# Kernel tuning notes

Hardware: AMD Instinct MI355X
Metric: run time of the kernel (lower is better)

Reference implementation:

```python
import jax, jax.numpy as jnp
import numpy as np

NUM_HEADS = 12
TOPK = 4


def setup_inputs() -> dict:
    key = jax.random.key(0)
    ks = jax.random.split(key, 5)
    B, N, C = 32, 577, 768
    s = 0.02
    return {
        "x": jax.random.normal(ks[0], (B, N, C), jnp.float32),
        "qkv_w": jax.random.normal(ks[1], (3 * C, C), jnp.float32) * s,
        "qkv_b": jax.random.normal(ks[2], (3 * C,), jnp.float32) * s,
        "proj_w": jax.random.normal(ks[3], (C, C), jnp.float32) * s,
        "proj_b": jax.random.normal(ks[4], (C,), jnp.float32) * s,
    }


def reference(x, qkv_w, qkv_b, proj_w, proj_b):
    B, N, C = x.shape
    H = NUM_HEADS
    D = C // H
    scale = D ** -0.5  # 0.125, matches original_attention.scale

    # qkv projection: (B,N,3C) -> (3,B,H,N,D)
    qkv = (x @ qkv_w.T + qkv_b).reshape(B, N, 3, H, D).transpose(2, 0, 3, 1, 4)
    q, k, v = qkv[0], qkv[1], qkv[2]

    # heuristic head routing: mean squared query energy per head
    scores = jnp.mean(q.astype(jnp.float32) ** 2, axis=(0, 2, 3))  # (H,)
    _, idx = jax.lax.top_k(scores, TOPK)
    idx = jnp.sort(idx)  # (topk,)

    q_sel = q[:, idx]  # (B,topk,N,D)
    k_sel = k[:, idx]
    v_sel = v[:, idx]

    attn = jax.nn.softmax(jnp.einsum('bhnd,bhmd->bhnm', q_sel, k_sel) * scale, axis=-1)
    y_sel = jnp.einsum('bhnm,bhmd->bhnd', attn, v_sel)  # (B,topk,N,D)

    # scatter selected heads back into full-size tensors (as in the torch module)
    y_full = jnp.zeros((B, H, N, D), x.dtype).at[:, idx].set(y_sel)
    x_out = y_full.transpose(0, 2, 1, 3).reshape(B, N, C) @ proj_w.T + proj_b

    attn_full = jnp.zeros((B, H, N, N), x.dtype).at[:, idx].set(attn)
    return x_out, attn_full
```

## Files before the change

### kernel.cpp

```cpp
#include <hip/hip_runtime.h>
#include <hip/hip_bf16.h>
#include <stdint.h>
#include <stddef.h>

#define B_ 32
#define N_ 577
#define C_ 768
#define H_ 12
#define D_ 64
#define M_ (B_*N_)
#define K3_ (3*C_)
#define NP_ 640
#define NN_ (N_*N_)

typedef __bf16 bf16x8_t __attribute__((ext_vector_type(8)));
typedef float f32x4 __attribute__((ext_vector_type(4)));
typedef unsigned short u16x8 __attribute__((ext_vector_type(8)));
typedef unsigned short u16x4 __attribute__((ext_vector_type(4)));

static __device__ __forceinline__ f32x4 mfma16(u16x8 a, u16x8 b, f32x4 c) {
  return __builtin_amdgcn_mfma_f32_16x16x32_bf16(
      __builtin_bit_cast(bf16x8_t, a), __builtin_bit_cast(bf16x8_t, b), c, 0, 0, 0);
}

static __device__ __forceinline__ unsigned short f2bf(float x) {
  unsigned int u = __builtin_bit_cast(unsigned int, x);
  u += 0x7fffu + ((u >> 16) & 1u);
  return (unsigned short)(u >> 16);
}

static __device__ __forceinline__ void glds16(const unsigned short* g, unsigned short* l) {
  __builtin_amdgcn_global_load_lds(
      (__attribute__((address_space(1))) void*)g,
      (__attribute__((address_space(3))) void*)l,
      16, 0, 0);
}

__global__ void k_cvt(const float* __restrict__ src, unsigned short* __restrict__ dst, int n4,
                      float* __restrict__ zeroptr) {
  if (zeroptr && blockIdx.x == 0 && threadIdx.x < 16) zeroptr[threadIdx.x] = 0.f;
  int stride = gridDim.x * blockDim.x;
  for (int i = blockIdx.x * blockDim.x + threadIdx.x; i < n4; i += stride) {
    float4 v = ((const float4*)src)[i];
    u16x4 o;
    o[0] = f2bf(v.x); o[1] = f2bf(v.y); o[2] = f2bf(v.z); o[3] = f2bf(v.w);
    *(u16x4*)(dst + (size_t)i * 4) = o;
  }
}

template<int MODE>
__global__ void k_gemm(const unsigned short* __restrict__ A,
                       const unsigned short* __restrict__ Bm,
                       const float* __restrict__ bias,
                       unsigned short* __restrict__ qb,
                       unsigned short* __restrict__ kb,
                       unsigned short* __restrict__ vb,
                       float* __restrict__ scores,
                       float* __restrict__ out,
                       int Mtot, int Ktot)
{
  __shared__ unsigned short As[128 * 32];
  __shared__ unsigned short Bs[128 * 32];
  const int bm = blockIdx.x, bn = blockIdx.y;
  const int tid = threadIdx.x;
  const int w = tid >> 6, l = tid & 63;
  const int wm = w >> 1, wn = w & 1;
  const int lr = l & 15, lg = l >> 4;
  const int lk = lg * 8;
  f32x4 acc[4][4] = {};
  const int rowA0 = bm * 128, rowB0 = bn * 128;
  const int le0 = w * 1024 + l * 8;
  const int kiters = Ktot >> 5;
  for (int kt = 0; kt < kiters; ++kt) {
    __syncthreads();
    #pragma unroll
    for (int c = 0; c < 2; ++c) {
      int lea = le0 + c * 512;
      int ra = lea >> 5, ka = lea & 31;
      glds16(A  + (size_t)(rowA0 + ra) * Ktot + kt * 32 + ka, As + (w * 2 + c) * 512);
      glds16(Bm + (size_t)(rowB0 + ra) * Ktot + kt * 32 + ka, Bs + (w * 2 + c) * 512);
    }
    __syncthreads();
    u16x8 af[4], bfr[4];
    #pragma unroll
    for (int i = 0; i < 4; ++i)
      af[i] = *(const u16x8*)(As + (wm * 64 + i * 16 + lr) * 32 + lk);
    #pragma unroll
    for (int j = 0; j < 4; ++j)
      bfr[j] = *(const u16x8*)(Bs + (wn * 64 + j * 16 + lr) * 32 + lk);
    #pragma unroll
    for (int i = 0; i < 4; ++i)
      #pragma unroll
      for (int j = 0; j < 4; ++j)
        acc[i][j] = mfma16(af[i], bfr[j], acc[i][j]);
  }

  const int rbase = lg * 4;
  if (MODE == 0) {
    const int n0 = rowB0 + wn * 64;
    const int t0 = n0 / C_;
    const int h0 = (n0 % C_) >> 6;
    unsigned short* dstbuf = (t0 == 0) ? qb : ((t0 == 1) ? kb : vb);
    float bs[4];
    #pragma unroll
    for (int j = 0; j < 4; ++j) bs[j] = bias[n0 + j * 16 + lr];
    float sq = 0.f;
    #pragma unroll
    for (int i = 0; i < 4; ++i) {
      const int mbase = rowA0 + wm * 64 + i * 16 + rbase;
      const int bb0 = mbase / N_;
      const int np0 = mbase - bb0 * N_;
      #pragma unroll
      for (int r = 0; r < 4; ++r) {
        const int mm = mbase + r;
        if (mm < Mtot) {
          int np = np0 + r, bb = bb0;
          if (np >= N_) { np -= N_; bb += 1; }
          unsigned short* drow = dstbuf + (((size_t)(bb * H_ + h0)) * N_ + np) * D_;
          #pragma unroll
          for (int j = 0; j < 4; ++j) {
            const float v = acc[i][j][r] + bs[j];
            if (t0 == 0) sq += v * v;
            drow[j * 16 + lr] = f2bf(v);
          }
        }
      }
    }
    if (t0 == 0) {
      #pragma unroll
      for (int s2 = 1; s2 < 64; s2 <<= 1) sq += __shfl_xor(sq, s2);
      if (l == 0) atomicAdd(scores + h0, sq);
    }
  } else {
    #pragma unroll
    for (int j = 0; j < 4; ++j) {
      const int n = rowB0 + wn * 64 + j * 16 + lr;
      const float bsj = bias[n];
      #pragma unroll
      for (int i = 0; i < 4; ++i) {
        const int mbase = rowA0 + wm * 64 + i * 16 + rbase;
        #pragma unroll
        for (int r = 0; r < 4; ++r) {
          const int mm = mbase + r;
          if (mm < Mtot) out[(size_t)mm * C_ + n] = acc[i][j][r] + bsj;
        }
      }
    }
  }
}

__global__ void k_topk(const float* __restrict__ scores, int* __restrict__ idxp) {
  if (threadIdx.x == 0 && blockIdx.x == 0) {
    float s[H_];
    bool used[H_];
    for (int i = 0; i < H_; ++i) { s[i] = scores[i]; used[i] = false; }
    int sel[4];
    for (int t = 0; t < 4; ++t) {
      int best = 0; float bv = -3.0e38f;
      for (int i = 0; i < H_; ++i)
        if (!used[i] && s[i] > bv) { bv = s[i]; best = i; }
      used[best] = true; sel[t] = best;
    }
    for (int a = 0; a < 4; ++a)
      for (int b = a + 1; b < 4; ++b)
        if (sel[b] < sel[a]) { int t = sel[a]; sel[a] = sel[b]; sel[b] = t; }
    for (int t = 0; t < 4; ++t) idxp[t] = sel[t];
  }
}

__global__ void k_gatherpw(const float* __restrict__ pw, const int* __restrict__ idxp,
                           unsigned short* __restrict__ pwsel) {
  int i = blockIdx.x * 256 + threadIdx.x;
  if (i >= C_ * 256) return;
  int c = i >> 8, j = i & 255;
  int h = idxp[j >> 6], d = j & 63;
  pwsel[i] = f2bf(pw[(size_t)c * C_ + h * 64 + d]);
}

__global__ void k_transv(const unsigned short* __restrict__ vb, unsigned short* __restrict__ vT) {
  __shared__ unsigned short t[64][72];
  const int bid = blockIdx.x;
  const int nt = bid % 10;
  const int bh = bid / 10;
  const int n0 = nt * 64;
  const int tid = threadIdx.x;
  {
    const int r = tid >> 2, q4 = (tid & 3) * 16;
    const int n = n0 + r;
    u16x8 v0, v1;
    if (n < N_) {
      const unsigned short* src = vb + ((size_t)bh * N_ + n) * D_ + q4;
      v0 = *(const u16x8*)(src);
      v1 = *(const u16x8*)(src + 8);
    } else {
      #pragma unroll
      for (int j = 0; j < 8; ++j) { v0[j] = 0; v1[j] = 0; }
    }
    *(u16x8*)&t[r][q4] = v0;
    *(u16x8*)&t[r][q4 + 8] = v1;
  }
  __syncthreads();
  {
    const int d = tid >> 2, nc = (tid & 3) * 16;
    u16x8 w0, w1;
    #pragma unroll
    for (int j = 0; j < 8; ++j) { w0[j] = t[nc + j][d]; w1[j] = t[nc + 8 + j][d]; }
    unsigned short* dst = vT + ((size_t)bh * D_ + d) * NP_ + n0 + nc;
    *(u16x8*)(dst) = w0;
    *(u16x8*)(dst + 8) = w1;
  }
}

#define ZSEG_ 41617
__global__ void k_attn(const unsigned short* __restrict__ qb,
                       const unsigned short* __restrict__ kb,
                       const unsigned short* __restrict__ vT,
                       const int* __restrict__ idxp,
                       float* __restrict__ attn_out,
                       unsigned short* __restrict__ ysel)
{
  __shared__ unsigned short Plds[4][16][72];
  const int bid = blockIdx.x;

  if (bid >= 1280) {
    const int zbid = bid - 1280;
    const int seg = zbid & 7, zp = zbid >> 3;
    const int zb = zp >> 3, hu = zp & 7;
    const int i0 = idxp[0], i1 = idxp[1], i2 = idxp[2], i3 = idxp[3];
    int zh = 0, u = 0;
    for (int c = 0; c < H_; ++c) {
      bool sel = (c == i0) | (c == i1) | (c == i2) | (c == i3);
      if (!sel) { if (u == hu) { zh = c; break; } ++u; }
    }
    float* slab = attn_out + ((size_t)(zb * H_ + zh)) * NN_ + seg * ZSEG_;
    const int len = (seg == 7) ? (NN_ - 7 * ZSEG_) : ZSEG_;
    for (int t = threadIdx.x * 4; t < len; t += 4096) {
      #pragma unroll
      for (int j = 0; j < 4; ++j)
        if (t + j < len) slab[t + j] = 0.f;
    }
    return;
  }

  const int qt = bid >> 7;
  const int pair = bid & 127;
  const int b  = pair >> 2;
  const int hs = pair & 3;
  const int h  = idxp[hs];
  const int tid = threadIdx.x;
  const int w = tid >> 6, l = tid & 63;
  const int lr = l & 15, lg = l >> 4, lk = lg * 8;
  const float sc2 = 0.125f * 1.44269504f;

  const size_t bh = (size_t)(b * H_ + h);
  const unsigned short* qbase = qb + bh * ((size_t)N_ * D_);
  const unsigned short* kbase = kb + bh * ((size_t)N_ * D_);
  const unsigned short* vbase = vT + bh * ((size_t)D_ * NP_);
  float* aout = attn_out + bh * (size_t)NN_;

  const int qrow = qt * 64 + w * 16 + lr;
  const int qrc = (qrow < N_) ? qrow : (N_ - 1);
  u16x8 qf0 = *(const u16x8*)(qbase + (size_t)qrc * D_ + lk);
  u16x8 qf1 = *(const u16x8*)(qbase + (size_t)qrc * D_ + 32 + lk);

  float m2[4], lsum[4];
  #pragma unroll
  for (int r = 0; r < 4; ++r) { m2[r] = -1.0e30f; lsum[r] = 0.f; }

  for (int kt = 0; kt < 10; ++kt) {
    f32x4 s[4];
    bool vc[4];
    #pragma unroll
    for (int cg = 0; cg < 4; ++cg) {
      const int kc = kt * 64 + cg * 16 + lr;
      vc[cg] = (kc < N_);
      const int kcc = vc[cg] ? kc : (N_ - 1);
      const unsigned short* kp = kbase + (size_t)kcc * D_;
      u16x8 k0 = *(const u16x8*)(kp + lk);
      u16x8 k1 = *(const u16x8*)(kp + 32 + lk);
      f32x4 a = {0.f, 0.f, 0.f, 0.f};
      __builtin_amdgcn_s_setprio(1);
      a = mfma16(qf0, k0, a);
      a = mfma16(qf1, k1, a);
      __builtin_amdgcn_s_setprio(0);
      s[cg] = a;
    }
    #pragma unroll
    for (int r = 0; r < 4; ++r) {
      float tk[4];
      float mk = -1.0e30f;
      #pragma unroll
      for (int cg = 0; cg < 4; ++cg) {
        tk[cg] = vc[cg] ? s[cg][r] * sc2 : -1.0e30f;
        mk = fmaxf(mk, tk[cg]);
      }
      const float mn = fmaxf(m2[r], mk);
      float se = 0.f;
      #pragma unroll
      for (int cg = 0; cg < 4; ++cg)
        se += exp2f(tk[cg] - mn);
      lsum[r] = lsum[r] * exp2f(m2[r] - mn) + se;
      m2[r] = mn;
    }
  }
  #pragma unroll
  for (int x = 1; x < 16; x <<= 1) {
    #pragma unroll
    for (int r = 0; r < 4; ++r) {
      const float mo = __shfl_xor(m2[r], x);
      const float lo = __shfl_xor(lsum[r], x);
      const float mn = fmaxf(m2[r], mo);
      lsum[r] = lsum[r] * exp2f(m2[r] - mn) + lo * exp2f(mo - mn);
      m2[r] = mn;
    }
  }
  float off2[4];
  #pragma unroll
  for (int r = 0; r < 4; ++r) off2[r] = m2[r] + __log2f(lsum[r]);

  f32x4 y[4] = {};
  const int orow0 = qt * 64 + w * 16 + lg * 4;

  for (int kt = 0; kt < 10; ++kt) {
    f32x4 s[4];
    bool vc[4];
    #pragma unroll
    for (int cg = 0; cg < 4; ++cg) {
      const int kc = kt * 64 + cg * 16 + lr;
      vc[cg] = (kc < N_);
      const int kcc = vc[cg] ? kc : (N_ - 1);
      const unsigned short* kp = kbase + (size_t)kcc * D_;
      u16x8 k0 = *(const u16x8*)(kp + lk);
      u16x8 k1 = *(const u16x8*)(kp + 32 + lk);
      f32x4 a = {0.f, 0.f, 0.f, 0.f};
      __builtin_amdgcn_s_setprio(1);
      a = mfma16(qf0, k0, a);
      a = mfma16(qf1, k1, a);
      __builtin_amdgcn_s_setprio(0);
      s[cg] = a;
    }
    #pragma unroll
    for (int cg = 0; cg < 4; ++cg) {
      const int kc = kt * 64 + cg * 16 + lr;
      #pragma unroll
      for (int r = 0; r < 4; ++r) {
        float p = exp2f(__builtin_fmaf(s[cg][r], sc2, -off2[r]));
        p = vc[cg] ? p : 0.f;
        const int row = orow0 + r;
        if (vc[cg] && row < N_)
          aout[(size_t)row * N_ + kc] = p;
        Plds[w][lg * 4 + r][cg * 16 + lr] = f2bf(p);
      }
    }
    u16x8 pa0 = *(const u16x8*)&Plds[w][lr][lk];
    u16x8 pa1 = *(const u16x8*)&Plds[w][lr][32 + lk];
    #pragma unroll
    for (int cg2 = 0; cg2 < 4; ++cg2) {
      const unsigned short* vp = vbase + (size_t)(cg2 * 16 + lr) * NP_ + kt * 64;
      u16x8 v0 = *(const u16x8*)(vp + lk);
      u16x8 v1 = *(const u16x8*)(vp + 32 + lk);
      __builtin_amdgcn_s_setprio(1);
      y[cg2] = mfma16(pa0, v0, y[cg2]);
      y[cg2] = mfma16(pa1, v1, y[cg2]);
      __builtin_amdgcn_s_setprio(0);
    }
  }

  #pragma unroll
  for (int cg2 = 0; cg2 < 4; ++cg2)
    #pragma unroll
    for (int r = 0; r < 4; ++r) {
      const int row = orow0 + r;
      if (row < N_)
        ysel[((size_t)(b * N_ + row)) * 256 + hs * 64 + cg2 * 16 + lr] = f2bf(y[cg2][r]);
    }
}

extern "C" void kernel_launch(void* const* d_in, const int* in_sizes, int n_in,
                              void* d_out, int out_size, void* d_ws, size_t ws_size,
                              hipStream_t stream) {
  const float* x      = (const float*)d_in[0];
  const float* qkv_w  = (const float*)d_in[1];
  const float* qkv_b  = (const float*)d_in[2];
  const float* proj_w = (const float*)d_in[3];
  const float* proj_b = (const float*)d_in[4];

  float* xout = (float*)d_out;
  float* attn_out = (float*)d_out + (size_t)M_ * C_;

  char* ws = (char*)d_ws;
  size_t o = 0;
  unsigned short* xb    = (unsigned short*)(ws + o);
  unsigned short* vT    = (unsigned short*)(ws + o);
  o += 31457280;
  unsigned short* wqkvb = (unsigned short*)(ws + o); o += 3538944;
  unsigned short* qb    = (unsigned short*)(ws + o); o += 28360704;
  unsigned short* kb    = (unsigned short*)(ws + o); o += 28360704;
  unsigned short* vb    = (unsigned short*)(ws + o); o += 28360704;
  unsigned short* ysel  = (unsigned short*)(ws + o); o += 9453568;
  unsigned short* pwsel = (unsigned short*)(ws + o); o += 393216;
  float* scores         = (float*)(ws + o);
  int*   idxp           = (int*)(ws + o + 64);

  k_cvt<<<2048, 256, 0, stream>>>(x, xb, (M_ * C_) / 4, scores);
  k_cvt<<<1728, 256, 0, stream>>>(qkv_w, wqkvb, (K3_ * C_) / 4, nullptr);

  k_gemm<0><<<dim3(145, 18), 256, 0, stream>>>(xb, wqkvb, qkv_b,
                                               qb, kb, vb, scores, nullptr,
                                               M_, C_);

  k_topk<<<1, 64, 0, stream>>>(scores, idxp);
  k_gatherpw<<<768, 256, 0, stream>>>(proj_w, idxp, pwsel);
  k_transv<<<3840, 256, 0, stream>>>(vb, vT);

  k_attn<<<3328, 256, 0, stream>>>(qb, kb, vT, idxp, attn_out, ysel);

  k_gemm<1><<<dim3(145, 6), 256, 0, stream>>>(ysel, pwsel, proj_b,
                                              nullptr, nullptr, nullptr, nullptr, xout,
                                              M_, 256);
}
```

Measured before the change: 389.6 us.

## Move attention zero-fill into QKV GEMM and transpose only selected V heads

```diff
diff --git a/kernel.cpp b/kernel.cpp
--- a/kernel.cpp
+++ b/kernel.cpp
@@ -48,6 +48,8 @@
   }
 }
 
+#define ZROWS_ 6
+#define ZPER_ 146948
 template<int MODE>
 __global__ void k_gemm(const unsigned short* __restrict__ A,
                        const unsigned short* __restrict__ Bm,
@@ -61,8 +63,23 @@
 {
   __shared__ unsigned short As[128 * 32];
   __shared__ unsigned short Bs[128 * 32];
-  const int bm = blockIdx.x, bn = blockIdx.y;
   const int tid = threadIdx.x;
+
+  if (MODE == 0 && blockIdx.y < ZROWS_) {
+    const int zblk = blockIdx.y * 145 + blockIdx.x;
+    const size_t Z = (size_t)B_ * H_ * NN_;
+    size_t s0 = (size_t)zblk * ZPER_;
+    size_t len = ZPER_;
+    if (s0 + len > Z) len = Z - s0;
+    float* zo = out + s0;
+    const float4 z4 = {0.f, 0.f, 0.f, 0.f};
+    for (size_t t = tid * 4; t + 4 <= len; t += 4096)
+      *(float4*)(zo + t) = z4;
+    return;
+  }
+
+  const int bm = blockIdx.x;
+  const int bn = (MODE == 0) ? (blockIdx.y - ZROWS_) : blockIdx.y;
   const int w = tid >> 6, l = tid & 63;
   const int wm = w >> 1, wn = w & 1;
   const int lr = l & 15, lg = l >> 4;
@@ -177,11 +194,16 @@
   pwsel[i] = f2bf(pw[(size_t)c * C_ + h * 64 + d]);
 }
 
-__global__ void k_transv(const unsigned short* __restrict__ vb, unsigned short* __restrict__ vT) {
+__global__ void k_transv(const unsigned short* __restrict__ vb, unsigned short* __restrict__ vT,
+                         const int* __restrict__ idxp) {
   __shared__ unsigned short t[64][72];
   const int bid = blockIdx.x;
   const int nt = bid % 10;
-  const int bh = bid / 10;
+  const int p  = bid / 10;
+  const int b  = p >> 2, hs = p & 3;
+  const int h  = idxp[hs];
+  const size_t bh_src = (size_t)(b * H_ + h);
+  const size_t bh_dst = (size_t)(b * 4 + hs);
   const int n0 = nt * 64;
   const int tid = threadIdx.x;
   {
@@ -189,7 +211,7 @@
     const int n = n0 + r;
     u16x8 v0, v1;
     if (n < N_) {
-      const unsigned short* src = vb + ((size_t)bh * N_ + n) * D_ + q4;
+      const unsigned short* src = vb + (bh_src * N_ + n) * D_ + q4;
       v0 = *(const u16x8*)(src);
       v1 = *(const u16x8*)(src + 8);
     } else {
@@ -205,13 +227,12 @@
     u16x8 w0, w1;
     #pragma unroll
     for (int j = 0; j < 8; ++j) { w0[j] = t[nc + j][d]; w1[j] = t[nc + 8 + j][d]; }
-    unsigned short* dst = vT + ((size_t)bh * D_ + d) * NP_ + n0 + nc;
+    unsigned short* dst = vT + (bh_dst * D_ + d) * NP_ + n0 + nc;
     *(u16x8*)(dst) = w0;
     *(u16x8*)(dst + 8) = w1;
   }
 }
 
-#define ZSEG_ 41617
 __global__ void k_attn(const unsigned short* __restrict__ qb,
                        const unsigned short* __restrict__ kb,
                        const unsigned short* __restrict__ vT,
@@ -222,26 +243,6 @@
   __shared__ unsigned short Plds[4][16][72];
   const int bid = blockIdx.x;
 
-  if (bid >= 1280) {
-    const int zbid = bid - 1280;
-    const int seg = zbid & 7, zp = zbid >> 3;
-    const int zb = zp >> 3, hu = zp & 7;
-    const int i0 = idxp[0], i1 = idxp[1], i2 = idxp[2], i3 = idxp[3];
-    int zh = 0, u = 0;
-    for (int c = 0; c < H_; ++c) {
-      bool sel = (c == i0) | (c == i1) | (c == i2) | (c == i3);
-      if (!sel) { if (u == hu) { zh = c; break; } ++u; }
-    }
-    float* slab = attn_out + ((size_t)(zb * H_ + zh)) * NN_ + seg * ZSEG_;
-    const int len = (seg == 7) ? (NN_ - 7 * ZSEG_) : ZSEG_;
-    for (int t = threadIdx.x * 4; t < len; t += 4096) {
-      #pragma unroll
-      for (int j = 0; j < 4; ++j)
-        if (t + j < len) slab[t + j] = 0.f;
-    }
-    return;
-  }
-
   const int qt = bid >> 7;
   const int pair = bid & 127;
   const int b  = pair >> 2;
@@ -255,7 +256,7 @@
   const size_t bh = (size_t)(b * H_ + h);
   const unsigned short* qbase = qb + bh * ((size_t)N_ * D_);
   const unsigned short* kbase = kb + bh * ((size_t)N_ * D_);
-  const unsigned short* vbase = vT + bh * ((size_t)D_ * NP_);
+  const unsigned short* vbase = vT + (size_t)(b * 4 + hs) * ((size_t)D_ * NP_);
   float* aout = attn_out + bh * (size_t)NN_;
 
   const int qrow = qt * 64 + w * 16 + lr;
@@ -405,15 +406,15 @@
   k_cvt<<<2048, 256, 0, stream>>>(x, xb, (M_ * C_) / 4, scores);
   k_cvt<<<1728, 256, 0, stream>>>(qkv_w, wqkvb, (K3_ * C_) / 4, nullptr);
 
-  k_gemm<0><<<dim3(145, 18), 256, 0, stream>>>(xb, wqkvb, qkv_b,
-                                               qb, kb, vb, scores, nullptr,
+  k_gemm<0><<<dim3(145, 18 + ZROWS_), 256, 0, stream>>>(xb, wqkvb, qkv_b,
+                                               qb, kb, vb, scores, attn_out,
                                                M_, C_);
 
   k_topk<<<1, 64, 0, stream>>>(scores, idxp);
   k_gatherpw<<<768, 256, 0, stream>>>(proj_w, idxp, pwsel);
-  k_transv<<<3840, 256, 0, stream>>>(vb, vT);
-
-  k_attn<<<3328, 256, 0, stream>>>(qb, kb, vT, idxp, attn_out, ysel);
+  k_transv<<<1280, 256, 0, stream>>>(vb, vT, idxp);
+
+  k_attn<<<1280, 256, 0, stream>>>(qb, kb, vT, idxp, attn_out, ysel);
 
   k_gemm<1><<<dim3(145, 6), 256, 0, stream>>>(ysel, pwsel, proj_b,
                                               nullptr, nullptr, nullptr, nullptr, xout,
```

Result: faster. 376.9 us (-3.2%).
